# Optimization experiments

Measured on AMD Instinct MI355X. Metric: run time of the kernel, lower is better.

## Reference

```python
import jax, jax.numpy as jnp
import numpy as np
from jax import lax

S, B, V, H = 2048, 64, 32000, 1024


def setup_inputs() -> dict:
    key = jax.random.key(0)
    ks = jax.random.split(key, 8)
    scale = 1.0 / np.sqrt(H)
    return {
        "input": jax.random.randint(ks[0], (S, B), 0, V, dtype=jnp.int64),  # [S,B] tokens
        "emb": jax.random.normal(ks[1], (V, H), jnp.float32) * scale,
        "W_ih": jax.random.normal(ks[2], (H, H), jnp.float32) * scale,
        "W_hh": jax.random.normal(ks[3], (H, H), jnp.float32) * scale,
        "b_ih": jax.random.normal(ks[4], (H,), jnp.float32) * scale,
        "b_hh": jax.random.normal(ks[5], (H,), jnp.float32) * scale,
        "W_fc": jax.random.normal(ks[6], (2, H), jnp.float32) * scale,
        "b_fc": jax.random.normal(ks[7], (2,), jnp.float32) * scale,
    }


def reference(input, emb, W_ih, W_hh, b_ih, b_hh, W_fc, b_fc):
    # Embedding lookup: [S,B] -> [S,B,H]
    x = emb[input]
    # Precompute input projections for all timesteps in one big GEMM: [S,B,H]
    xp = jnp.einsum('sbh,kh->sbk', x, W_ih) + b_ih
    h0 = jnp.zeros((input.shape[1], W_hh.shape[0]), dtype=emb.dtype)

    def step(h, xp_t):
        h = jnp.tanh(xp_t + h @ W_hh.T + b_hh)  # Elman cell
        return h, None

    h_final, _ = lax.scan(step, h0, xp)
    # Classifier on final hidden state: [B,2]
    return h_final @ W_fc.T + b_fc
```

## Files before the change

kernel.cpp:

```cpp
#include <hip/hip_runtime.h>
#include <hip/hip_fp16.h>

#define S_LEN 2048
#define BATCH 64
#define VOC   32000
#define HID   1024

typedef __attribute__((ext_vector_type(4))) float          f32x4;
typedef __attribute__((ext_vector_type(8))) _Float16       half8;

union PunH { uint4 u; half8 h; };

__global__ void prep_kernel(const float* __restrict__ emb,
                            const float* __restrict__ wih,
                            const float* __restrict__ whh,
                            __half* __restrict__ embh,
                            __half* __restrict__ wihh,
                            unsigned short* __restrict__ whh_hi,
                            unsigned short* __restrict__ whh_lo,
                            unsigned short* __restrict__ hbuf,
                            unsigned int* __restrict__ zbuf,
                            int* __restrict__ flags)
{
    long i = (long)blockIdx.x * blockDim.x + threadIdx.x;
    if (i < (long)VOC * HID) embh[i] = __float2half(emb[i]);
    if (i < (long)HID * HID) {
        wihh[i] = __float2half(wih[i]);
        float wv = whh[i];
        __half hi = __float2half(wv);
        __half lo = __float2half(wv - __half2float(hi));
        whh_hi[i] = __half_as_ushort(hi);
        whh_lo[i] = __half_as_ushort(lo);
    }
    if (i < BATCH * HID) hbuf[i] = 0;
    if (i < 512) flags[i] = 0;
    if (i < 256) zbuf[i] = 0u;
}

__global__ void __launch_bounds__(256)
xp_gemm(const int* __restrict__ tok,
        const __half* __restrict__ embh,
        const __half* __restrict__ wihh,
        const float* __restrict__ b_ih,
        __half* __restrict__ xp)
{
    __shared__ __half Asm[128][72];
    __shared__ __half Bsm[128][72];
    __shared__ int toks[128];

    const int tid   = threadIdx.x;
    const int ntile = blockIdx.x;
    const int mtile = blockIdx.y;

    if (tid < 128) {
        int t = tok[mtile * 128 + tid];
        toks[tid] = (t < 0) ? 0 : (t >= VOC ? VOC - 1 : t);
    }
    __syncthreads();

    const int lane = tid & 63, wv = tid >> 6;
    const int mv = (wv & 1) * 64, nv = (wv >> 1) * 64;

    f32x4 acc[4][4];
    #pragma unroll
    for (int a = 0; a < 4; a++)
        #pragma unroll
        for (int b = 0; b < 4; b++) acc[a][b] = (f32x4)0.0f;

    const int srow = tid & 127;
    const int shalf = (tid >> 7) * 32;
    const __half* gA = embh + (size_t)toks[srow] * HID + shalf;
    const __half* gB = wihh + (size_t)(ntile * 128 + srow) * HID + shalf;

    for (int kb = 0; kb < 16; kb++) {
        const uint4* pa = (const uint4*)(gA + kb * 64);
        const uint4* pb = (const uint4*)(gB + kb * 64);
        uint4 va0 = pa[0], va1 = pa[1], va2 = pa[2], va3 = pa[3];
        uint4 vb0 = pb[0], vb1 = pb[1], vb2 = pb[2], vb3 = pb[3];
        uint4* la = (uint4*)&Asm[srow][shalf];
        uint4* lb = (uint4*)&Bsm[srow][shalf];
        la[0] = va0; la[1] = va1; la[2] = va2; la[3] = va3;
        lb[0] = vb0; lb[1] = vb1; lb[2] = vb2; lb[3] = vb3;
        __syncthreads();

        #pragma unroll
        for (int ks = 0; ks < 2; ks++) {
            half8 af[4], bf[4];
            const int kc = ks * 32 + (lane >> 4) * 8;
            #pragma unroll
            for (int m = 0; m < 4; m++)
                af[m] = *(const half8*)&Asm[mv + m * 16 + (lane & 15)][kc];
            #pragma unroll
            for (int n = 0; n < 4; n++)
                bf[n] = *(const half8*)&Bsm[nv + n * 16 + (lane & 15)][kc];
            #pragma unroll
            for (int m = 0; m < 4; m++)
                #pragma unroll
                for (int n = 0; n < 4; n++)
                    acc[m][n] = __builtin_amdgcn_mfma_f32_16x16x32_f16(
                        af[m], bf[n], acc[m][n], 0, 0, 0);
        }
        __syncthreads();
    }

    #pragma unroll
    for (int n = 0; n < 4; n++) {
        const int ng = ntile * 128 + nv + n * 16 + (lane & 15);
        const float bi = b_ih[ng];
        const int wg = ng >> 5, kk = ng & 31;
        #pragma unroll
        for (int m = 0; m < 4; m++) {
            #pragma unroll
            for (int i = 0; i < 4; i++) {
                const int mg = mtile * 128 + mv + m * 16 + (lane >> 4) * 4 + i;
                const int s = mg >> 6, b = mg & 63;
                const size_t off = ((size_t)(s * 8 + (b >> 3)) * 32 + wg) * 256
                                 + (b & 7) * 32 + kk;
                xp[off] = __float2half(acc[m][n][i] + bi);
            }
        }
    }
}

__global__ void __launch_bounds__(256, 1)
recur_kernel(const __half* __restrict__ xp,
             const unsigned short* __restrict__ whh_hi,
             const unsigned short* __restrict__ whh_lo,
             const float* __restrict__ b_hh,
             unsigned short* hbuf,
             const unsigned int* zbuf, int* flags)
{
    extern __shared__ char smem[];
    float*  red  = (float*)(smem + 131072);
    __half* ring = (__half*)(smem + 135168);

    const int tid  = threadIdx.x;
    const int lane = tid & 63;
    const int wv   = tid >> 6;
    const int g    = blockIdx.x >> 5;
    const int w    = blockIdx.x & 31;

    {
        const int r  = tid >> 3;
        const int c0 = (tid & 7) * 128;
        const unsigned short* ghi = whh_hi + (size_t)(w * 32 + r) * HID + c0;
        const unsigned short* glo = whh_lo + (size_t)(w * 32 + r) * HID + c0;
        #pragma unroll
        for (int j = 0; j < 16; j++) {
            uint4 vhi = ((const uint4*)ghi)[j];
            uint4 vlo = ((const uint4*)glo)[j];
            int byte = r * 2048 + c0 * 2 + j * 16;
            byte ^= (r & 7) << 4;
            *(uint4*)(smem + byte)         = vhi;
            *(uint4*)(smem + 65536 + byte) = vlo;
        }
    }
    uint4 xn_next;
    if (wv == 0 && tid < 32) {
        const size_t b0 = ((size_t)g * 32 + w) * 256;
        uint4 v0 = ((const uint4*)(xp + b0))[tid];
        *(uint4*)&ring[tid * 8] = v0;
        xn_next = ((const uint4*)(xp + ((size_t)(8 + g) * 32 + (size_t)w) * 256))[tid];
    }
    __syncthreads();

    const bool act = (lane & 15) < 8;
    const int  ar  = lane & 15;
    const int  ak  = (lane >> 4) * 8;
    const float bhh = b_hh[w * 32 + (tid & 31)];
    int* const myflag = flags + g * 32 + w;

    for (int t = 0; t < S_LEN; t++) {
        if (lane < 32) {
            const int* fp = flags + g * 32 + lane;
            int fv, spin = 0;
            do {
                asm volatile("global_load_dword %0, %1, off sc0 sc1\n\t"
                             "s_waitcnt vmcnt(0)"
                             : "=v"(fv) : "v"(fp) : "memory");
            } while (fv < t && ++spin < 4096);
        }
        if (wv == 0 && tid < 32 && t + 1 < S_LEN)
            *(uint4*)&ring[((t + 1) & 1) * 256 + tid * 8] = xn_next;

        const size_t hoff = (size_t)(t & 3) * (BATCH * HID)
                          + (size_t)(g * 8 + (act ? ar : 0)) * HID + wv * 256 + ak;
        const unsigned short* ph = act ? (hbuf + hoff) : (const unsigned short*)zbuf;
        uint4 c[8];
        asm volatile(
            "global_load_dwordx4 %0, %8, off sc0 sc1\n\t"
            "global_load_dwordx4 %1, %8, off offset:64 sc0 sc1\n\t"
            "global_load_dwordx4 %2, %8, off offset:128 sc0 sc1\n\t"
            "global_load_dwordx4 %3, %8, off offset:192 sc0 sc1\n\t"
            "global_load_dwordx4 %4, %8, off offset:256 sc0 sc1\n\t"
            "global_load_dwordx4 %5, %8, off offset:320 sc0 sc1\n\t"
            "global_load_dwordx4 %6, %8, off offset:384 sc0 sc1\n\t"
            "global_load_dwordx4 %7, %8, off offset:448 sc0 sc1\n\t"
            "s_waitcnt vmcnt(0)"
            : "=&v"(c[0]), "=&v"(c[1]), "=&v"(c[2]), "=&v"(c[3]),
              "=&v"(c[4]), "=&v"(c[5]), "=&v"(c[6]), "=&v"(c[7])
            : "v"(ph)
            : "memory");

        if (wv == 0 && tid < 32 && t + 2 < S_LEN)
            xn_next = ((const uint4*)(xp
                + ((size_t)((t + 2) * 8 + g) * 32 + (size_t)w) * 256))[tid];

        f32x4 acc_h[2], acc_l[2];
        #pragma unroll
        for (int j = 0; j < 2; j++) {
            acc_h[j] = (f32x4)0.0f; acc_l[j] = (f32x4)0.0f;
        }
        const int kbyte0 = (wv * 256 + ak) * 2;
        #pragma unroll
        for (int kk = 0; kk < 8; kk++) {
            PunH pa; pa.u = c[kk];
            const half8 af = pa.h;
            #pragma unroll
            for (int j = 0; j < 2; j++) {
                const int rloc = j * 16 + (lane & 15);
                int bb = rloc * 2048 + kbyte0 + kk * 64;
                bb ^= (rloc & 7) << 4;
                PunH pbh; pbh.u = *(const uint4*)(smem + bb);
                PunH pbl; pbl.u = *(const uint4*)(smem + 65536 + bb);
                acc_h[j] = __builtin_amdgcn_mfma_f32_16x16x32_f16(af, pbh.h, acc_h[j], 0, 0, 0);
                acc_l[j] = __builtin_amdgcn_mfma_f32_16x16x32_f16(af, pbl.h, acc_l[j], 0, 0, 0);
            }
        }

        if (lane < 32) {
            #pragma unroll
            for (int j = 0; j < 2; j++) {
                const f32x4 d = acc_h[j] + acc_l[j];
                const int col = j * 16 + (lane & 15);
                #pragma unroll
                for (int i = 0; i < 4; i++) {
                    const int r = (lane >> 4) * 4 + i;
                    red[(wv * 8 + r) * 32 + col] = d[i];
                }
            }
        }
        __syncthreads();

        {
            const int r = tid >> 5, n = tid & 31;
            float z = red[r * 32 + n] + red[(8 + r) * 32 + n]
                    + red[(16 + r) * 32 + n] + red[(24 + r) * 32 + n];
            z += __half2float(ring[(t & 1) * 256 + tid]) + bhh;
            const float h = tanhf(z);
            const unsigned int hv = __half_as_ushort(__float2half(h));
            const size_t off = (size_t)((t + 1) & 3) * (BATCH * HID)
                             + (size_t)(g * 8 + r) * HID + w * 32 + n;
            asm volatile("global_store_short %0, %1, off sc0 sc1\n\t"
                         "s_waitcnt vmcnt(0)"
                         :: "v"(hbuf + off), "v"(hv) : "memory");
        }
        __syncthreads();
        if (tid == 0) {
            const int fv = t + 1;
            asm volatile("global_store_dword %0, %1, off sc0 sc1"
                         :: "v"(myflag), "v"(fv) : "memory");
        }
    }
}

__global__ void cls_kernel(const unsigned short* __restrict__ hbuf,
                           const float* __restrict__ wfc,
                           const float* __restrict__ bfc,
                           float* __restrict__ out)
{
    const int b = blockIdx.x, lane = threadIdx.x;
    const unsigned short* hp = hbuf + (size_t)b * HID;
    float p0 = 0.f, p1 = 0.f;
    for (int k = lane; k < HID; k += 64) {
        const float h = __half2float(__ushort_as_half(hp[k]));
        p0 += h * wfc[k];
        p1 += h * wfc[HID + k];
    }
    #pragma unroll
    for (int s = 32; s; s >>= 1) {
        p0 += __shfl_down(p0, s);
        p1 += __shfl_down(p1, s);
    }
    if (lane == 0) {
        out[b * 2 + 0] = p0 + bfc[0];
        out[b * 2 + 1] = p1 + bfc[1];
    }
}

extern "C" void kernel_launch(void* const* d_in, const int* in_sizes, int n_in,
                              void* d_out, int out_size, void* d_ws, size_t ws_size,
                              hipStream_t stream)
{
    const int*   tok = (const int*)d_in[0];
    const float* emb = (const float*)d_in[1];
    const float* wih = (const float*)d_in[2];
    const float* whh = (const float*)d_in[3];
    const float* bih = (const float*)d_in[4];
    const float* bhh = (const float*)d_in[5];
    const float* wfc = (const float*)d_in[6];
    const float* bfc = (const float*)d_in[7];
    float* out = (float*)d_out;

    char* ws = (char*)d_ws;
    size_t off = 0;
    auto alloc = [&](size_t bytes) {
        char* p = ws + off;
        off += (bytes + 255) & ~(size_t)255;
        return p;
    };
    __half*         xp      = (__half*)alloc((size_t)S_LEN * BATCH * HID * 2);
    __half*         embh    = (__half*)alloc((size_t)VOC * HID * 2);
    __half*         wihh    = (__half*)alloc((size_t)HID * HID * 2);
    unsigned short* whh_hi  = (unsigned short*)alloc((size_t)HID * HID * 2);
    unsigned short* whh_lo  = (unsigned short*)alloc((size_t)HID * HID * 2);
    unsigned short* hbuf    = (unsigned short*)alloc((size_t)4 * BATCH * HID * 2);
    unsigned int*   zbuf    = (unsigned int*)alloc(1024);
    int*            flags   = (int*)alloc(2048);

    if (off > ws_size) {
        hipMemsetAsync(d_out, 0, (size_t)out_size * sizeof(float), stream);
        return;
    }

    prep_kernel<<<dim3((VOC * HID) / 256), 256, 0, stream>>>(
        emb, wih, whh, embh, wihh, whh_hi, whh_lo, hbuf, zbuf, flags);

    xp_gemm<<<dim3(8, 1024), 256, 0, stream>>>(tok, embh, wihh, bih, xp);

    const unsigned int shmem = 136192;
    hipFuncSetAttribute(reinterpret_cast<const void*>(recur_kernel),
                        hipFuncAttributeMaxDynamicSharedMemorySize, (int)shmem);
    void* args[] = { (void*)&xp, (void*)&whh_hi, (void*)&whh_lo, (void*)&bhh,
                     (void*)&hbuf, (void*)&zbuf, (void*)&flags };
    hipLaunchCooperativeKernel(reinterpret_cast<const void*>(recur_kernel),
                               dim3(256), dim3(256), args, shmem, stream);

    cls_kernel<<<dim3(64), 64, 0, stream>>>(hbuf, wfc, bfc, out);
}
```

Before: 7.438 ms.

## Split each recurrence step into two half-batch phases with ping-pong flags

Each block's 8 batch rows are now handled as two halves of 4, alternating through 2*S phases with separate flag arrays A and B. While one half's flag wait and hidden-state load are in flight, the other half's MFMA and tanh can proceed, so global sync latency overlaps with compute. The hidden-state load is issued ahead and its waitcnt deferred, and the store no longer blocks on completion. The cost is twice as many barriers and flag polls per timestep, half-empty MFMA tiles, and a larger xp ring buffer.

```diff
diff --git a/kernel.cpp b/kernel.cpp
--- a/kernel.cpp
+++ b/kernel.cpp
@@ -10,6 +10,21 @@
 typedef __attribute__((ext_vector_type(8))) _Float16       half8;
 
 union PunH { uint4 u; half8 h; };
+
+#define ISSUE_HLOAD(c, ph)                                                   \
+    asm volatile(                                                            \
+        "global_load_dwordx4 %0, %8, off sc0 sc1\n\t"                        \
+        "global_load_dwordx4 %1, %8, off offset:64 sc0 sc1\n\t"              \
+        "global_load_dwordx4 %2, %8, off offset:128 sc0 sc1\n\t"             \
+        "global_load_dwordx4 %3, %8, off offset:192 sc0 sc1\n\t"             \
+        "global_load_dwordx4 %4, %8, off offset:256 sc0 sc1\n\t"             \
+        "global_load_dwordx4 %5, %8, off offset:320 sc0 sc1\n\t"             \
+        "global_load_dwordx4 %6, %8, off offset:384 sc0 sc1\n\t"             \
+        "global_load_dwordx4 %7, %8, off offset:448 sc0 sc1"                 \
+        : "=&v"(c[0]), "=&v"(c[1]), "=&v"(c[2]), "=&v"(c[3]),                \
+          "=&v"(c[4]), "=&v"(c[5]), "=&v"(c[6]), "=&v"(c[7])                 \
+        : "v"(ph)                                                            \
+        : "memory")
 
 __global__ void prep_kernel(const float* __restrict__ emb,
                             const float* __restrict__ wih,
@@ -162,49 +177,37 @@
         *(uint4*)&ring[tid * 8] = v0;
         xn_next = ((const uint4*)(xp + ((size_t)(8 + g) * 32 + (size_t)w) * 256))[tid];
     }
-    __syncthreads();
-
-    const bool act = (lane & 15) < 8;
+
+    const bool act = (lane & 15) < 4;
     const int  ar  = lane & 15;
     const int  ak  = (lane >> 4) * 8;
     const float bhh = b_hh[w * 32 + (tid & 31)];
-    int* const myflag = flags + g * 32 + w;
-
-    for (int t = 0; t < S_LEN; t++) {
-        if (lane < 32) {
-            const int* fp = flags + g * 32 + lane;
-            int fv, spin = 0;
-            do {
-                asm volatile("global_load_dword %0, %1, off sc0 sc1\n\t"
-                             "s_waitcnt vmcnt(0)"
-                             : "=v"(fv) : "v"(fp) : "memory");
-            } while (fv < t && ++spin < 4096);
-        }
-        if (wv == 0 && tid < 32 && t + 1 < S_LEN)
-            *(uint4*)&ring[((t + 1) & 1) * 256 + tid * 8] = xn_next;
-
-        const size_t hoff = (size_t)(t & 3) * (BATCH * HID)
-                          + (size_t)(g * 8 + (act ? ar : 0)) * HID + wv * 256 + ak;
-        const unsigned short* ph = act ? (hbuf + hoff) : (const unsigned short*)zbuf;
-        uint4 c[8];
-        asm volatile(
-            "global_load_dwordx4 %0, %8, off sc0 sc1\n\t"
-            "global_load_dwordx4 %1, %8, off offset:64 sc0 sc1\n\t"
-            "global_load_dwordx4 %2, %8, off offset:128 sc0 sc1\n\t"
-            "global_load_dwordx4 %3, %8, off offset:192 sc0 sc1\n\t"
-            "global_load_dwordx4 %4, %8, off offset:256 sc0 sc1\n\t"
-            "global_load_dwordx4 %5, %8, off offset:320 sc0 sc1\n\t"
-            "global_load_dwordx4 %6, %8, off offset:384 sc0 sc1\n\t"
-            "global_load_dwordx4 %7, %8, off offset:448 sc0 sc1\n\t"
-            "s_waitcnt vmcnt(0)"
-            : "=&v"(c[0]), "=&v"(c[1]), "=&v"(c[2]), "=&v"(c[3]),
-              "=&v"(c[4]), "=&v"(c[5]), "=&v"(c[6]), "=&v"(c[7])
-            : "v"(ph)
-            : "memory");
-
-        if (wv == 0 && tid < 32 && t + 2 < S_LEN)
-            xn_next = ((const uint4*)(xp
-                + ((size_t)((t + 2) * 8 + g) * 32 + (size_t)w) * 256))[tid];
+    int* const flagsA = flags;
+    int* const flagsB = flags + 256;
+
+    uint4 c[8];
+    {
+        const unsigned short* ph = act
+            ? (hbuf + (size_t)(g * 8 + ar) * HID + wv * 256 + ak)
+            : (const unsigned short*)zbuf;
+        ISSUE_HLOAD(c, ph);
+    }
+    __syncthreads();
+
+    for (int p = 0; p < 2 * S_LEN; p++) {
+        const int X = p & 1;
+        const int t = p >> 1;
+
+        if (X == 0) {
+            if (wv == 0 && tid < 32 && t + 1 < S_LEN)
+                *(uint4*)&ring[((t + 1) & 3) * 256 + tid * 8] = xn_next;
+            if (wv == 0 && tid < 32 && t + 2 < S_LEN)
+                xn_next = ((const uint4*)(xp
+                    + ((size_t)((t + 2) * 8 + g) * 32 + (size_t)w) * 256))[tid];
+        }
+
+        asm volatile("s_waitcnt vmcnt(0)" ::: "memory");
+        __builtin_amdgcn_sched_barrier(0);
 
         f32x4 acc_h[2], acc_l[2];
         #pragma unroll
@@ -242,24 +245,46 @@
         }
         __syncthreads();
 
-        {
+        if (tid < 128) {
             const int r = tid >> 5, n = tid & 31;
             float z = red[r * 32 + n] + red[(8 + r) * 32 + n]
                     + red[(16 + r) * 32 + n] + red[(24 + r) * 32 + n];
-            z += __half2float(ring[(t & 1) * 256 + tid]) + bhh;
+            z += __half2float(ring[(t & 3) * 256 + X * 128 + tid]) + bhh;
             const float h = tanhf(z);
-            const unsigned int hv = __half_as_ushort(__float2half(h));
+            const unsigned int hv = (unsigned int)__half_as_ushort(__float2half(h));
             const size_t off = (size_t)((t + 1) & 3) * (BATCH * HID)
-                             + (size_t)(g * 8 + r) * HID + w * 32 + n;
-            asm volatile("global_store_short %0, %1, off sc0 sc1\n\t"
-                         "s_waitcnt vmcnt(0)"
+                             + (size_t)(g * 8 + X * 4 + r) * HID + w * 32 + n;
+            asm volatile("global_store_short %0, %1, off sc0 sc1"
                          :: "v"(hbuf + off), "v"(hv) : "memory");
         }
+
+        const int  need = (X == 0) ? t : t + 1;
+        const int* pf   = ((X == 0) ? flagsB : flagsA) + g * 32;
+        if (lane < 32) {
+            const int* fp = pf + lane;
+            int fv, spin = 0;
+            do {
+                asm volatile("global_load_dword %0, %1, off sc0 sc1\n\t"
+                             "s_waitcnt vmcnt(0)"
+                             : "=v"(fv) : "v"(fp) : "memory");
+            } while (fv < need && ++spin < 4096);
+        }
         __syncthreads();
+
         if (tid == 0) {
+            int* mf = ((X == 0) ? flagsA : flagsB) + g * 32 + w;
             const int fv = t + 1;
             asm volatile("global_store_dword %0, %1, off sc0 sc1"
-                         :: "v"(myflag), "v"(fv) : "memory");
+                         :: "v"(mf), "v"(fv) : "memory");
+        }
+
+        if (p + 1 < 2 * S_LEN) {
+            const unsigned short* ph = act
+                ? (hbuf + (size_t)(need & 3) * (BATCH * HID)
+                       + (size_t)(g * 8 + (X == 0 ? 4 : 0) + ar) * HID
+                       + wv * 256 + ak)
+                : (const unsigned short*)zbuf;
+            ISSUE_HLOAD(c, ph);
         }
     }
 }
@@ -328,7 +353,7 @@
 
     xp_gemm<<<dim3(8, 1024), 256, 0, stream>>>(tok, embh, wihh, bih, xp);
 
-    const unsigned int shmem = 136192;
+    const unsigned int shmem = 137216;
     hipFuncSetAttribute(reinterpret_cast<const void*>(recur_kernel),
                         hipFuncAttributeMaxDynamicSharedMemorySize, (int)shmem);
     void* args[] = { (void*)&xp, (void*)&whh_hi, (void*)&whh_lo, (void*)&bhh,
```

Result: slower. 11.11 ms (+49.4%).
